# Performance work log

Hardware: AMD Instinct MI355X
Metric: run time of the kernel (lower is better)

The kernel has to match this reference:

```python
import jax, jax.numpy as jnp
from jax import lax
import numpy as np

H = 512       # nhidden
IN = 300      # title/body input dim
TLEN = 40     # title_len
BLEN = 200    # body_len
B = 256       # batch
CH = 512      # classify_hidden
NC = 4        # nclass


def setup_inputs():
    key = jax.random.key(0)
    ks = jax.random.split(key, 17)
    s = 1.0 / np.sqrt(H)
    u = lambda k, sh: jax.random.uniform(k, sh, jnp.float32, -s, s)
    return {
        "x": jax.random.normal(ks[0], (B, TLEN + BLEN, IN), jnp.float32),
        "title_Wih": u(ks[1], (2, 4 * H, IN)),
        "title_Whh": u(ks[2], (2, 4 * H, H)),
        "title_bih": u(ks[3], (2, 4 * H)),
        "title_bhh": u(ks[4], (2, 4 * H)),
        "body_Wih": u(ks[5], (2, 4 * H, IN)),
        "body_Whh": u(ks[6], (2, 4 * H, H)),
        "body_bih": u(ks[7], (2, 4 * H)),
        "body_bhh": u(ks[8], (2, 4 * H)),
        "bil_W": u(ks[9], (1, 2 * H, 2 * H)),
        "bil_b": u(ks[10], (1,)),
        "attn_W": u(ks[11], (2 * H, 4 * H)),
        "attn_b": u(ks[12], (2 * H,)),
        "dec_W": u(ks[13], (CH, 4 * H)),
        "dec_b": u(ks[14], (CH,)),
        "cls_W": u(ks[15], (NC, CH)),
        "cls_b": u(ks[16], (NC,)),
    }


def _lstm_dir(x, Wih, Whh, bih, bhh, h0, c0, reverse):
    # x: [B, T, I]; precompute input-to-gate contributions for all timesteps
    xg = jnp.einsum('bti,gi->btg', x, Wih) + bih + bhh  # [B, T, 4H]

    def step(carry, xg_t):
        h, c = carry
        g = xg_t + h @ Whh.T  # PyTorch gate order: i, f, g, o
        i, f, gg, o = jnp.split(g, 4, axis=-1)
        c = jax.nn.sigmoid(f) * c + jax.nn.sigmoid(i) * jnp.tanh(gg)
        h = jax.nn.sigmoid(o) * jnp.tanh(c)
        return (h, c), h

    (hT, cT), hs = lax.scan(step, (h0, c0), jnp.swapaxes(xg, 0, 1), reverse=reverse)
    return jnp.swapaxes(hs, 0, 1), hT, cT  # outputs aligned to input time order


def _bilstm(x, Wih, Whh, bih, bhh, h0, c0):
    # h0, c0: [2, B, H] (dir 0 = forward, dir 1 = backward)
    out_f, hf, cf = _lstm_dir(x, Wih[0], Whh[0], bih[0], bhh[0], h0[0], c0[0], False)
    out_b, hb, cb = _lstm_dir(x, Wih[1], Whh[1], bih[1], bhh[1], h0[1], c0[1], True)
    out = jnp.concatenate([out_f, out_b], axis=-1)  # [B, T, 2H]
    return out, jnp.stack([hf, hb]), jnp.stack([cf, cb])


def reference(x, title_Wih, title_Whh, title_bih, title_bhh,
              body_Wih, body_Whh, body_bih, body_bhh,
              bil_W, bil_b, attn_W, attn_b, dec_W, dec_b, cls_W, cls_b):
    title, body = x[:, :TLEN, :], x[:, TLEN:, :]
    z = jnp.zeros((2, x.shape[0], H), x.dtype)
    title_out, hn, cn = _bilstm(title, title_Wih, title_Whh, title_bih, title_bhh, z, z)
    # conditional=True: body RNN starts from title final (h, c)
    body_out, _, _ = _bilstm(body, body_Wih, body_Whh, body_bih, body_bhh, hn, cn)
    body_last = body_out[:, -1, :]  # [B, 2H]
    # vectorized bilinear attention over title timesteps (replaces per-t loop)
    scores = jnp.einsum('bte,oeh,bh->bto', title_out, bil_W, body_last) + bil_b
    scores = jax.nn.softmax(scores[..., 0], axis=-1)  # [B, TLEN]
    context = jnp.einsum('bte,bt->be', title_out, scores)  # [B, 2H]
    attn = jnp.tanh(jnp.concatenate([context, body_last], axis=1) @ attn_W.T + attn_b)
    output = jnp.concatenate([title_out[:, -1, :], attn], axis=1)  # [B, 4H]
    class_hidden = output @ dec_W.T + dec_b  # dropout p=0.0 -> identity
    return jax.nn.softmax(class_hidden @ cls_W.T + cls_b, axis=-1)
```

## Files before the change

kernel.cpp:

```cpp
#include <hip/hip_runtime.h>
#include <math.h>

#define HD    512
#define BATCH 256
#define TDIM  240
#define INDIM 300

typedef unsigned short u16;
typedef u16   u16x8 __attribute__((ext_vector_type(8)));
typedef float f32x4 __attribute__((ext_vector_type(4)));

__device__ __forceinline__ u16 bf16_rte(float v) {
    unsigned u = __builtin_bit_cast(unsigned, v);
    unsigned r = (u + 0x7FFFu + ((u >> 16) & 1u)) >> 16;
    return (u16)r;
}

__device__ __forceinline__ void mfma16(f32x4& d, u16x8 a, u16x8 b) {
    asm("v_mfma_f32_16x16x32_bf16 %0, %1, %2, %0" : "+v"(d) : "v"(a), "v"(b));
}

__global__ __launch_bounds__(256) void split_pad(
    const float* __restrict__ src, u16* __restrict__ hi, u16* __restrict__ lo,
    int rows, int kin, int kout)
{
    long i = (long)blockIdx.x * 256 + threadIdx.x;
    if (i >= (long)rows * kout) return;
    int r = (int)(i / kout);
    int k = (int)(i - (long)r * kout);
    float v = (k < kin) ? src[(long)r * kin + k] : 0.f;
    u16 h = bf16_rte(v);
    float hf = __builtin_bit_cast(float, (unsigned)h << 16);
    hi[i] = h;
    lo[i] = bf16_rte(v - hf);
}

struct StepDir {
    const u16* Wih_h; const u16* Wih_l;
    const u16* Whh_h; const u16* Whh_l;
    const float* bih; const float* bhh;
    const u16* hh; const u16* hl;
    u16* oh; u16* ol;
    float* c;
    float* ex; long exs;
    int t;
};

__global__ __launch_bounds__(64) void step_mfma(
    const u16* __restrict__ xh, const u16* __restrict__ xl,
    StepDir d0, StepDir d1)
{
    StepDir D = blockIdx.z ? d1 : d0;
    const int gx   = blockIdx.x;
    const int xcd  = gx & 7, j = gx >> 3;
    const int cblk = xcd * 4 + (j & 3);
    const int rblk = j >> 2;
    const int lane = threadIdx.x;
    const int lr   = lane & 15;
    const int lk8  = (lane >> 4) * 8;
    const int b0   = rblk * 32;
    const int col  = cblk * 16 + lr;

    f32x4 acc[2][4];
    #pragma unroll
    for (int g = 0; g < 4; ++g) {
        float bs = D.bih[g * HD + col] + D.bhh[g * HD + col];
        acc[0][g] = f32x4{bs, bs, bs, bs};
        acc[1][g] = f32x4{bs, bs, bs, bs};
    }

    u16x8 Ah0[2], Al0[2], Bh0[4], Bl0[4];
    u16x8 Ah1[2], Al1[2], Bh1[4], Bl1[4];

    auto MMA = [&](u16x8 (&Ah)[2], u16x8 (&Al)[2], u16x8 (&Bh)[4], u16x8 (&Bl)[4]) {
        #pragma unroll
        for (int rt = 0; rt < 2; ++rt)
            #pragma unroll
            for (int g = 0; g < 4; ++g) {
                mfma16(acc[rt][g], Ah[rt], Bh[g]);
                mfma16(acc[rt][g], Ah[rt], Bl[g]);
                mfma16(acc[rt][g], Al[rt], Bh[g]);
            }
    };

    {
        auto LD = [&](u16x8 (&Ah)[2], u16x8 (&Al)[2], u16x8 (&Bh)[4], u16x8 (&Bl)[4], int ks) {
            const int ko = ks * 32 + lk8;
            #pragma unroll
            for (int rt = 0; rt < 2; ++rt) {
                long off = ((long)(b0 + rt * 16 + lr) * TDIM + D.t) * 320 + ko;
                Ah[rt] = *(const u16x8*)(xh + off);
                Al[rt] = *(const u16x8*)(xl + off);
            }
            #pragma unroll
            for (int g = 0; g < 4; ++g) {
                long off = (long)(g * HD + col) * 320 + ko;
                Bh[g] = *(const u16x8*)(D.Wih_h + off);
                Bl[g] = *(const u16x8*)(D.Wih_l + off);
            }
        };
        LD(Ah0, Al0, Bh0, Bl0, 0);
        #pragma unroll
        for (int ks = 0; ks < 10; ks += 2) {
            LD(Ah1, Al1, Bh1, Bl1, ks + 1);
            MMA(Ah0, Al0, Bh0, Bl0);
            if (ks + 2 < 10) LD(Ah0, Al0, Bh0, Bl0, ks + 2);
            MMA(Ah1, Al1, Bh1, Bl1);
        }
    }
    {
        auto LD = [&](u16x8 (&Ah)[2], u16x8 (&Al)[2], u16x8 (&Bh)[4], u16x8 (&Bl)[4], int ks) {
            const int ko = ks * 32 + lk8;
            #pragma unroll
            for (int rt = 0; rt < 2; ++rt) {
                long off = (long)(b0 + rt * 16 + lr) * HD + ko;
                Ah[rt] = *(const u16x8*)(D.hh + off);
                Al[rt] = *(const u16x8*)(D.hl + off);
            }
            #pragma unroll
            for (int g = 0; g < 4; ++g) {
                long off = (long)(g * HD + col) * HD + ko;
                Bh[g] = *(const u16x8*)(D.Whh_h + off);
                Bl[g] = *(const u16x8*)(D.Whh_l + off);
            }
        };
        LD(Ah0, Al0, Bh0, Bl0, 0);
        #pragma unroll
        for (int ks = 0; ks < 16; ks += 2) {
            LD(Ah1, Al1, Bh1, Bl1, ks + 1);
            MMA(Ah0, Al0, Bh0, Bl0);
            if (ks + 2 < 16) LD(Ah0, Al0, Bh0, Bl0, ks + 2);
            MMA(Ah1, Al1, Bh1, Bl1);
        }
    }

    #pragma unroll
    for (int rt = 0; rt < 2; ++rt) {
        #pragma unroll
        for (int r = 0; r < 4; ++r) {
            const int b = b0 + rt * 16 + (lane >> 4) * 4 + r;
            const long hoff = (long)b * HD + col;
            float iv = acc[rt][0][r];
            float fv = acc[rt][1][r];
            float gv = acc[rt][2][r];
            float ov = acc[rt][3][r];
            float cp = D.c[hoff];
            float si = 1.f / (1.f + expf(-iv));
            float sf = 1.f / (1.f + expf(-fv));
            float so = 1.f / (1.f + expf(-ov));
            float cn = sf * cp + si * tanhf(gv);
            float hn = so * tanhf(cn);
            D.c[hoff] = cn;
            u16 hb = bf16_rte(hn);
            D.oh[hoff] = hb;
            D.ol[hoff] = bf16_rte(hn - __builtin_bit_cast(float, (unsigned)hb << 16));
            if (D.ex) D.ex[(long)b * D.exs + col] = hn;
        }
    }
}

__global__ __launch_bounds__(64) void xg_mfma(
    const u16* __restrict__ xh, const u16* __restrict__ xl,
    const u16* __restrict__ Wih_h, const u16* __restrict__ Wih_l,
    const float* __restrict__ bih, const float* __restrict__ bhh,
    float* __restrict__ xgT, int t0abs, int tstep)
{
    const int bx   = blockIdx.x;
    const int tloc = bx >> 9;
    const int rem  = bx & 511;
    const int rblk = rem >> 6;
    const int cgrp = rem & 63;
    const int lane = threadIdx.x;
    const int lr = lane & 15, lk8 = (lane >> 4) * 8;
    const int b0 = rblk * 32;
    const int tx = t0abs + tstep * tloc;
    const int colf0 = cgrp * 32 + lr;
    const int colf1 = colf0 + 16;

    f32x4 acc[2][2];
    {
        float bs0 = bih[colf0] + bhh[colf0];
        float bs1 = bih[colf1] + bhh[colf1];
        acc[0][0] = f32x4{bs0, bs0, bs0, bs0};
        acc[1][0] = f32x4{bs0, bs0, bs0, bs0};
        acc[0][1] = f32x4{bs1, bs1, bs1, bs1};
        acc[1][1] = f32x4{bs1, bs1, bs1, bs1};
    }

    u16x8 a0h[2], a0l[2], b0h[2], b0l[2];
    u16x8 a1h[2], a1l[2], b1h[2], b1l[2];

    auto LD = [&](u16x8 (&Ah)[2], u16x8 (&Al)[2], u16x8 (&Bh)[2], u16x8 (&Bl)[2], int ks) {
        const int ko = ks * 32 + lk8;
        #pragma unroll
        for (int rt = 0; rt < 2; ++rt) {
            long off = ((long)(b0 + rt * 16 + lr) * TDIM + tx) * 320 + ko;
            Ah[rt] = *(const u16x8*)(xh + off);
            Al[rt] = *(const u16x8*)(xl + off);
        }
        long w0 = (long)colf0 * 320 + ko;
        long w1 = (long)colf1 * 320 + ko;
        Bh[0] = *(const u16x8*)(Wih_h + w0);
        Bl[0] = *(const u16x8*)(Wih_l + w0);
        Bh[1] = *(const u16x8*)(Wih_h + w1);
        Bl[1] = *(const u16x8*)(Wih_l + w1);
    };
    auto MMA = [&](u16x8 (&Ah)[2], u16x8 (&Al)[2], u16x8 (&Bh)[2], u16x8 (&Bl)[2]) {
        #pragma unroll
        for (int rt = 0; rt < 2; ++rt)
            #pragma unroll
            for (int cf = 0; cf < 2; ++cf) {
                mfma16(acc[rt][cf], Ah[rt], Bh[cf]);
                mfma16(acc[rt][cf], Ah[rt], Bl[cf]);
                mfma16(acc[rt][cf], Al[rt], Bh[cf]);
            }
    };

    LD(a0h, a0l, b0h, b0l, 0);
    #pragma unroll
    for (int ks = 0; ks < 10; ks += 2) {
        LD(a1h, a1l, b1h, b1l, ks + 1);
        MMA(a0h, a0l, b0h, b0l);
        if (ks + 2 < 10) LD(a0h, a0l, b0h, b0l, ks + 2);
        MMA(a1h, a1l, b1h, b1l);
    }

    #pragma unroll
    for (int rt = 0; rt < 2; ++rt) {
        long o0 = ((long)tloc * 2048 + colf0) * 256 + b0 + rt * 16 + (lane >> 4) * 4;
        long o1 = ((long)tloc * 2048 + colf1) * 256 + b0 + rt * 16 + (lane >> 4) * 4;
        *(f32x4*)(xgT + o0) = acc[rt][0];
        *(f32x4*)(xgT + o1) = acc[rt][1];
    }
}

__device__ __forceinline__ void group_bar(unsigned* cnt, unsigned* gen,
                                          unsigned nb, unsigned g)
{
    __syncthreads();
    if (threadIdx.x == 0) {
        unsigned old = __hip_atomic_fetch_add(cnt, 1u, __ATOMIC_RELEASE,
                                              __HIP_MEMORY_SCOPE_AGENT);
        if (old == nb - 1u) {
            __hip_atomic_store(cnt, 0u, __ATOMIC_RELAXED, __HIP_MEMORY_SCOPE_AGENT);
            __hip_atomic_store(gen, g + 1u, __ATOMIC_RELEASE, __HIP_MEMORY_SCOPE_AGENT);
        } else {
            while (__hip_atomic_load(gen, __ATOMIC_RELAXED, __HIP_MEMORY_SCOPE_AGENT) < g + 1u)
                __builtin_amdgcn_s_sleep(2);
            (void)__hip_atomic_load(gen, __ATOMIC_ACQUIRE, __HIP_MEMORY_SCOPE_AGENT);
        }
    }
    __syncthreads();
}

__global__ __launch_bounds__(256) void lstm_persist(
    const float* __restrict__ xgT,
    const u16* __restrict__ Whh_h, const u16* __restrict__ Whh_l,
    u16* __restrict__ hAh, u16* __restrict__ hAl,
    u16* __restrict__ hBh, u16* __restrict__ hBl,
    float* __restrict__ cst,
    float* __restrict__ ex, long ex_bstride, int ex_t0, int ex_tstep,
    int ex_coff, int ex_final,
    unsigned* __restrict__ bars, int s0, int L)
{
    const int gx   = blockIdx.x;
    const int xcd  = gx & 7, j = gx >> 3;
    const int cblk = xcd * 4 + (j & 3);
    const int rblk = j >> 2;
    const int wid  = threadIdx.x >> 6;
    const int lane = threadIdx.x & 63;
    const int lr   = lane & 15;
    const int lk8  = (lane >> 4) * 8;
    const int b0   = rblk * 32;
    const int col  = cblk * 16 + lr;

    __shared__ u16 WH[64][520];
    __shared__ u16 WL[64][520];
    __shared__ f32x4 RED[3][64][8];

    for (int idx = threadIdx.x; idx < 64 * 64; idx += 256) {
        int rr = idx >> 6;
        int kk = (idx & 63) << 3;
        int g = rr >> 4, cc = rr & 15;
        long gro = (long)(g * HD + cblk * 16 + cc) * HD + kk;
        *(u16x8*)&WH[rr][kk] = *(const u16x8*)(Whh_h + gro);
        *(u16x8*)&WL[rr][kk] = *(const u16x8*)(Whh_l + gro);
    }
    __syncthreads();

    unsigned* bcnt = bars + rblk * 64;
    unsigned* bgen = bars + 512 + rblk * 64;
    unsigned gen = 0;
    const int ksbase = wid * 4;

    for (int ti = 0; ti < L; ++ti) {
        const int s = s0 + ti;
        const u16* hih = (s & 1) ? hBh : hAh;
        const u16* hil = (s & 1) ? hBl : hAl;
        u16* hoh = (s & 1) ? hAh : hBh;
        u16* hol = (s & 1) ? hAl : hBl;

        f32x4 acc[2][4];
        if (wid == 0) {
            #pragma unroll
            for (int rt = 0; rt < 2; ++rt)
                #pragma unroll
                for (int g = 0; g < 4; ++g) {
                    long o = ((long)ti * 2048 + g * HD + col) * 256
                             + b0 + rt * 16 + (lane >> 4) * 4;
                    acc[rt][g] = *(const f32x4*)(xgT + o);
                }
        } else {
            #pragma unroll
            for (int rt = 0; rt < 2; ++rt)
                #pragma unroll
                for (int g = 0; g < 4; ++g) acc[rt][g] = f32x4{0.f, 0.f, 0.f, 0.f};
        }

        u16x8 Ah0[2], Al0[2], Bh0[4], Bl0[4];
        u16x8 Ah1[2], Al1[2], Bh1[4], Bl1[4];

        auto MMA = [&](u16x8 (&Ah)[2], u16x8 (&Al)[2], u16x8 (&Bh)[4], u16x8 (&Bl)[4]) {
            #pragma unroll
            for (int rt = 0; rt < 2; ++rt)
                #pragma unroll
                for (int g = 0; g < 4; ++g) {
                    mfma16(acc[rt][g], Ah[rt], Bh[g]);
                    mfma16(acc[rt][g], Ah[rt], Bl[g]);
                    mfma16(acc[rt][g], Al[rt], Bh[g]);
                }
        };
        auto LD = [&](u16x8 (&Ah)[2], u16x8 (&Al)[2], u16x8 (&Bh)[4], u16x8 (&Bl)[4], int ks) {
            const int ko = ks * 32 + lk8;
            #pragma unroll
            for (int rt = 0; rt < 2; ++rt) {
                long off = (long)(b0 + rt * 16 + lr) * HD + ko;
                Ah[rt] = *(const u16x8*)(hih + off);
                Al[rt] = *(const u16x8*)(hil + off);
            }
            #pragma unroll
            for (int g = 0; g < 4; ++g) {
                Bh[g] = *(const u16x8*)&WH[g * 16 + lr][ko];
                Bl[g] = *(const u16x8*)&WL[g * 16 + lr][ko];
            }
        };

        LD(Ah0, Al0, Bh0, Bl0, ksbase + 0);
        LD(Ah1, Al1, Bh1, Bl1, ksbase + 1);
        MMA(Ah0, Al0, Bh0, Bl0);
        LD(Ah0, Al0, Bh0, Bl0, ksbase + 2);
        MMA(Ah1, Al1, Bh1, Bl1);
        LD(Ah1, Al1, Bh1, Bl1, ksbase + 3);
        MMA(Ah0, Al0, Bh0, Bl0);
        MMA(Ah1, Al1, Bh1, Bl1);

        if (wid != 0) {
            #pragma unroll
            for (int rt = 0; rt < 2; ++rt)
                #pragma unroll
                for (int g = 0; g < 4; ++g)
                    RED[wid - 1][lane][rt * 4 + g] = acc[rt][g];
        }
        __syncthreads();

        if (wid == 0) {
            #pragma unroll
            for (int w = 0; w < 3; ++w)
                #pragma unroll
                for (int rt = 0; rt < 2; ++rt)
                    #pragma unroll
                    for (int g = 0; g < 4; ++g)
                        acc[rt][g] += RED[w][lane][rt * 4 + g];

            const bool exw = (ex_final == -2) || (ex_final >= 0 && ti == ex_final);
            const int tt = ex_t0 + ex_tstep * ti;
            #pragma unroll
            for (int rt = 0; rt < 2; ++rt) {
                #pragma unroll
                for (int r = 0; r < 4; ++r) {
                    const int b = b0 + rt * 16 + (lane >> 4) * 4 + r;
                    const long hoff = (long)b * HD + col;
                    float iv = acc[rt][0][r];
                    float fv = acc[rt][1][r];
                    float gv = acc[rt][2][r];
                    float ov = acc[rt][3][r];
                    float cp = cst[hoff];
                    float si = 1.f / (1.f + expf(-iv));
                    float sf = 1.f / (1.f + expf(-fv));
                    float so = 1.f / (1.f + expf(-ov));
                    float cn = sf * cp + si * tanhf(gv);
                    float hn = so * tanhf(cn);
                    cst[hoff] = cn;
                    u16 hb = bf16_rte(hn);
                    hoh[hoff] = hb;
                    hol[hoff] = bf16_rte(hn - __builtin_bit_cast(float, (unsigned)hb << 16));
                    if (exw) ex[(long)b * ex_bstride + (long)tt * 1024 + ex_coff + col] = hn;
                }
            }
        }
        if (ti + 1 < L) { group_bar(bcnt, bgen, 32u, gen); ++gen; }
    }
}

__global__ __launch_bounds__(64) void body_persist(
    const u16* __restrict__ xh, const u16* __restrict__ xl,
    const u16* __restrict__ Wih_h, const u16* __restrict__ Wih_l,
    const u16* __restrict__ Whh_h, const u16* __restrict__ Whh_l,
    const float* __restrict__ bih, const float* __restrict__ bhh,
    u16* __restrict__ hAh, u16* __restrict__ hAl,
    u16* __restrict__ hBh, u16* __restrict__ hBl,
    float* __restrict__ cst, float* __restrict__ ex,
    unsigned* __restrict__ bars)
{
    const int gx   = blockIdx.x;
    const int xcd  = gx & 7, j = gx >> 3;
    const int cblk = xcd * 4 + (j & 3);
    const int rblk = j >> 2;
    const int lane = threadIdx.x;
    const int lr   = lane & 15;
    const int lk8  = (lane >> 4) * 8;
    const int b0   = rblk * 32;
    const int col  = cblk * 16 + lr;

    __shared__ u16 WH[64][520];
    __shared__ u16 WL[64][520];
    for (int idx = lane; idx < 64 * 64; idx += 64) {
        int rr = idx >> 6;
        int kk = (idx & 63) << 3;
        int g = rr >> 4, cc = rr & 15;
        long gro = (long)(g * HD + cblk * 16 + cc) * HD + kk;
        *(u16x8*)&WH[rr][kk] = *(const u16x8*)(Whh_h + gro);
        *(u16x8*)&WL[rr][kk] = *(const u16x8*)(Whh_l + gro);
    }
    __syncthreads();

    float bsum[4];
    #pragma unroll
    for (int g = 0; g < 4; ++g) bsum[g] = bih[g * HD + col] + bhh[g * HD + col];

    unsigned* bcnt = bars + rblk * 64;
    unsigned* bgen = bars + 512 + rblk * 64;
    unsigned gen = 0;

    for (int t = 1; t < 200; ++t) {
        const int s = 40 + t;
        const u16* hih = (s & 1) ? hBh : hAh;
        const u16* hil = (s & 1) ? hBl : hAl;
        u16* hoh = (s & 1) ? hAh : hBh;
        u16* hol = (s & 1) ? hAl : hBl;

        f32x4 acc[2][4];
        #pragma unroll
        for (int g = 0; g < 4; ++g) {
            acc[0][g] = f32x4{bsum[g], bsum[g], bsum[g], bsum[g]};
            acc[1][g] = f32x4{bsum[g], bsum[g], bsum[g], bsum[g]};
        }

        u16x8 Ah0[2], Al0[2], Bh0[4], Bl0[4];
        u16x8 Ah1[2], Al1[2], Bh1[4], Bl1[4];

        auto MMA = [&](u16x8 (&Ah)[2], u16x8 (&Al)[2], u16x8 (&Bh)[4], u16x8 (&Bl)[4]) {
            #pragma unroll
            for (int rt = 0; rt < 2; ++rt)
                #pragma unroll
                for (int g = 0; g < 4; ++g) {
                    mfma16(acc[rt][g], Ah[rt], Bh[g]);
                    mfma16(acc[rt][g], Ah[rt], Bl[g]);
                    mfma16(acc[rt][g], Al[rt], Bh[g]);
                }
        };
        {
            auto LD = [&](u16x8 (&Ah)[2], u16x8 (&Al)[2], u16x8 (&Bh)[4], u16x8 (&Bl)[4], int ks) {
                const int ko = ks * 32 + lk8;
                #pragma unroll
                for (int rt = 0; rt < 2; ++rt) {
                    long off = ((long)(b0 + rt * 16 + lr) * TDIM + (40 + t)) * 320 + ko;
                    Ah[rt] = *(const u16x8*)(xh + off);
                    Al[rt] = *(const u16x8*)(xl + off);
                }
                #pragma unroll
                for (int g = 0; g < 4; ++g) {
                    long off = (long)(g * HD + col) * 320 + ko;
                    Bh[g] = *(const u16x8*)(Wih_h + off);
                    Bl[g] = *(const u16x8*)(Wih_l + off);
                }
            };
            LD(Ah0, Al0, Bh0, Bl0, 0);
            #pragma unroll
            for (int ks = 0; ks < 10; ks += 2) {
                LD(Ah1, Al1, Bh1, Bl1, ks + 1);
                MMA(Ah0, Al0, Bh0, Bl0);
                if (ks + 2 < 10) LD(Ah0, Al0, Bh0, Bl0, ks + 2);
                MMA(Ah1, Al1, Bh1, Bl1);
            }
        }
        {
            auto LD = [&](u16x8 (&Ah)[2], u16x8 (&Al)[2], u16x8 (&Bh)[4], u16x8 (&Bl)[4], int ks) {
                const int ko = ks * 32 + lk8;
                #pragma unroll
                for (int rt = 0; rt < 2; ++rt) {
                    long off = (long)(b0 + rt * 16 + lr) * HD + ko;
                    Ah[rt] = *(const u16x8*)(hih + off);
                    Al[rt] = *(const u16x8*)(hil + off);
                }
                #pragma unroll
                for (int g = 0; g < 4; ++g) {
                    Bh[g] = *(const u16x8*)&WH[g * 16 + lr][ko];
                    Bl[g] = *(const u16x8*)&WL[g * 16 + lr][ko];
                }
            };
            LD(Ah0, Al0, Bh0, Bl0, 0);
            #pragma unroll
            for (int ks = 0; ks < 16; ks += 2) {
                LD(Ah1, Al1, Bh1, Bl1, ks + 1);
                MMA(Ah0, Al0, Bh0, Bl0);
                if (ks + 2 < 16) LD(Ah0, Al0, Bh0, Bl0, ks + 2);
                MMA(Ah1, Al1, Bh1, Bl1);
            }
        }
        float* exw = (t == 199) ? ex : (float*)nullptr;
        #pragma unroll
        for (int rt = 0; rt < 2; ++rt) {
            #pragma unroll
            for (int r = 0; r < 4; ++r) {
                const int b = b0 + rt * 16 + (lane >> 4) * 4 + r;
                const long hoff = (long)b * HD + col;
                float iv = acc[rt][0][r];
                float fv = acc[rt][1][r];
                float gv = acc[rt][2][r];
                float ov = acc[rt][3][r];
                float cp = cst[hoff];
                float si = 1.f / (1.f + expf(-iv));
                float sf = 1.f / (1.f + expf(-fv));
                float so = 1.f / (1.f + expf(-ov));
                float cn = sf * cp + si * tanhf(gv);
                float hn = so * tanhf(cn);
                cst[hoff] = cn;
                u16 hb = bf16_rte(hn);
                hoh[hoff] = hb;
                hol[hoff] = bf16_rte(hn - __builtin_bit_cast(float, (unsigned)hb << 16));
                if (exw) exw[(long)b * 1024 + col] = hn;
            }
        }
        group_bar(bcnt, bgen, 32u, gen);
        ++gen;
    }
}

template<int ACT>
__global__ __launch_bounds__(64) void mfma_gemm(
    const u16* __restrict__ Ah_, const u16* __restrict__ Al_,
    const u16* __restrict__ Wh_, const u16* __restrict__ Wl_,
    const float* __restrict__ bias, float* __restrict__ C,
    int ldc, int K, int n16)
{
    const int gx = blockIdx.x;
    const int nblk = gx % n16, mblk = gx / n16;
    const int lane = threadIdx.x;
    const int lr = lane & 15, lk8 = (lane >> 4) * 8;
    const int b0 = mblk * 32, col = nblk * 16 + lr;

    f32x4 acc[2] = {f32x4{0,0,0,0}, f32x4{0,0,0,0}};
    u16x8 A0[2], L0[2], A1[2], L1[2];
    u16x8 B0, M0, B1, M1;

    auto LD = [&](u16x8 (&A)[2], u16x8 (&L)[2], u16x8& B, u16x8& M, int ks) {
        const int ko = ks * 32 + lk8;
        #pragma unroll
        for (int rt = 0; rt < 2; ++rt) {
            long off = (long)(b0 + rt * 16 + lr) * K + ko;
            A[rt] = *(const u16x8*)(Ah_ + off);
            L[rt] = *(const u16x8*)(Al_ + off);
        }
        long woff = (long)col * K + ko;
        B = *(const u16x8*)(Wh_ + woff);
        M = *(const u16x8*)(Wl_ + woff);
    };
    auto MMA = [&](u16x8 (&A)[2], u16x8 (&L)[2], u16x8& B, u16x8& M) {
        #pragma unroll
        for (int rt = 0; rt < 2; ++rt) {
            mfma16(acc[rt], A[rt], B);
            mfma16(acc[rt], A[rt], M);
            mfma16(acc[rt], L[rt], B);
        }
    };

    const int NS = K >> 5;
    LD(A0, L0, B0, M0, 0);
    for (int ks = 0; ks < NS; ks += 2) {
        if (ks + 1 < NS) LD(A1, L1, B1, M1, ks + 1);
        MMA(A0, L0, B0, M0);
        if (ks + 2 < NS) LD(A0, L0, B0, M0, ks + 2);
        if (ks + 1 < NS) MMA(A1, L1, B1, M1);
    }

    float bs = bias ? bias[col] : 0.f;
    #pragma unroll
    for (int rt = 0; rt < 2; ++rt)
        #pragma unroll
        for (int r = 0; r < 4; ++r) {
            int m = b0 + rt * 16 + (lane >> 4) * 4 + r;
            float v = acc[rt][r] + bs;
            if (ACT == 1) v = tanhf(v);
            C[(long)m * ldc + col] = v;
        }
}

template<int BB>
__global__ __launch_bounds__(256) void lstm_step(
    const float* __restrict__ x,
    const float* __restrict__ Wih0, const float* __restrict__ Whh0,
    const float* __restrict__ bih0, const float* __restrict__ bhh0,
    const float* __restrict__ hin0, float* __restrict__ hnew0, float* __restrict__ cst0,
    float* __restrict__ ex0, int exs0, int tx0,
    const float* __restrict__ Wih1, const float* __restrict__ Whh1,
    const float* __restrict__ bih1, const float* __restrict__ bhh1,
    const float* __restrict__ hin1, float* __restrict__ hnew1, float* __restrict__ cst1,
    float* __restrict__ ex1, int exs1, int tx1)
{
    const int dir = blockIdx.z;
    const float* Wih = dir ? Wih1 : Wih0;
    const float* Whh = dir ? Whh1 : Whh0;
    const float* bih = dir ? bih1 : bih0;
    const float* bhh = dir ? bhh1 : bhh0;
    const float* hin = dir ? hin1 : hin0;
    float* hnew = dir ? hnew1 : hnew0;
    float* cst  = dir ? cst1  : cst0;
    float* ex   = dir ? ex1   : ex0;
    const int exs = dir ? exs1 : exs0;
    const int tx  = dir ? tx1  : tx0;

    const int bblk = blockIdx.x, kblk = blockIdx.y;
    const int tid = threadIdx.x;
    const int j  = tid & 15;
    const int ty = tid >> 4;
    const int k  = kblk * 16 + j;
    constexpr int RB = BB / 16;

    __shared__ float As[BB][33];
    __shared__ float Bs[32][65];

    float acc[RB][4];
    #pragma unroll
    for (int r = 0; r < RB; ++r)
        #pragma unroll
        for (int q = 0; q < 4; ++q) acc[r][q] = 0.f;

    const int lb = tid >> 5, lk = tid & 31;

    for (int kb = 0; kb < INDIM; kb += 32) {
        #pragma unroll
        for (int it = 0; it < BB/8; ++it) {
            int b = lb + it*8;
            int i = kb + lk;
            As[b][lk] = (i < INDIM) ? x[((bblk*BB + b)*TDIM + tx)*INDIM + i] : 0.f;
        }
        #pragma unroll
        for (int it = 0; it < 8; ++it) {
            int col = lb + it*8;
            int g = (col >> 4)*HD + kblk*16 + (col & 15);
            int i = kb + lk;
            Bs[lk][col] = (i < INDIM) ? Wih[g*INDIM + i] : 0.f;
        }
        __syncthreads();
        #pragma unroll
        for (int kk = 0; kk < 32; ++kk) {
            float a_[RB], b_[4];
            #pragma unroll
            for (int r = 0; r < RB; ++r) a_[r] = As[ty*RB + r][kk];
            #pragma unroll
            for (int q = 0; q < 4; ++q) b_[q] = Bs[kk][q*16 + j];
            #pragma unroll
            for (int r = 0; r < RB; ++r)
                #pragma unroll
                for (int q = 0; q < 4; ++q) acc[r][q] += a_[r]*b_[q];
        }
        __syncthreads();
    }
    for (int kb = 0; kb < HD; kb += 32) {
        #pragma unroll
        for (int it = 0; it < BB/8; ++it) {
            int b = lb + it*8;
            As[b][lk] = hin[(bblk*BB + b)*HD + kb + lk];
        }
        #pragma unroll
        for (int it = 0; it < 8; ++it) {
            int col = lb + it*8;
            int g = (col >> 4)*HD + kblk*16 + (col & 15);
            Bs[lk][col] = Whh[g*HD + kb + lk];
        }
        __syncthreads();
        #pragma unroll
        for (int kk = 0; kk < 32; ++kk) {
            float a_[RB], b_[4];
            #pragma unroll
            for (int r = 0; r < RB; ++r) a_[r] = As[ty*RB + r][kk];
            #pragma unroll
            for (int q = 0; q < 4; ++q) b_[q] = Bs[kk][q*16 + j];
            #pragma unroll
            for (int r = 0; r < RB; ++r)
                #pragma unroll
                for (int q = 0; q < 4; ++q) acc[r][q] += a_[r]*b_[q];
        }
        __syncthreads();
    }
    float bsum[4];
    #pragma unroll
    for (int q = 0; q < 4; ++q) bsum[q] = bih[q*HD + k] + bhh[q*HD + k];
    #pragma unroll
    for (int r = 0; r < RB; ++r) {
        int gb = bblk*BB + ty*RB + r;
        float iv = acc[r][0] + bsum[0];
        float fv = acc[r][1] + bsum[1];
        float gv = acc[r][2] + bsum[2];
        float ov = acc[r][3] + bsum[3];
        float cprev = cst[gb*HD + k];
        float si = 1.f/(1.f + expf(-iv));
        float sf = 1.f/(1.f + expf(-fv));
        float so = 1.f/(1.f + expf(-ov));
        float cn = sf*cprev + si*tanhf(gv);
        float hn = so*tanhf(cn);
        cst[gb*HD + k]  = cn;
        hnew[gb*HD + k] = hn;
        if (ex) ex[gb*exs + k] = hn;
    }
}

template<int ACT>
__global__ __launch_bounds__(256) void gemm_bias_act(
    const float* __restrict__ A, int lda,
    const float* __restrict__ W,
    const float* __restrict__ bias,
    float* __restrict__ C, int ldc,
    int K)
{
    const int mblk = blockIdx.x, nblk = blockIdx.y;
    const int tid = threadIdx.x;
    const int txd = tid & 15, ty = tid >> 4;
    __shared__ float As[32][33];
    __shared__ float Bs[32][65];
    float acc[2][4] = {{0.f,0.f,0.f,0.f},{0.f,0.f,0.f,0.f}};
    const int lb = tid >> 5, lk = tid & 31;

    for (int kb = 0; kb < K; kb += 32) {
        #pragma unroll
        for (int it = 0; it < 4; ++it) {
            int r = lb + it*8;
            As[r][lk] = A[(mblk*32 + r)*lda + kb + lk];
        }
        #pragma unroll
        for (int it = 0; it < 8; ++it) {
            int col = lb + it*8;
            Bs[lk][col] = W[(nblk*64 + col)*K + kb + lk];
        }
        __syncthreads();
        #pragma unroll
        for (int kk = 0; kk < 32; ++kk) {
            float a0 = As[ty*2 + 0][kk], a1 = As[ty*2 + 1][kk];
            float b_[4];
            #pragma unroll
            for (int q = 0; q < 4; ++q) b_[q] = Bs[kk][q*16 + txd];
            #pragma unroll
            for (int q = 0; q < 4; ++q) { acc[0][q] += a0*b_[q]; acc[1][q] += a1*b_[q]; }
        }
        __syncthreads();
    }
    #pragma unroll
    for (int r = 0; r < 2; ++r) {
        int m = mblk*32 + ty*2 + r;
        #pragma unroll
        for (int q = 0; q < 4; ++q) {
            int n = nblk*64 + q*16 + txd;
            float v = acc[r][q] + (bias ? bias[n] : 0.f);
            if (ACT == 1) v = tanhf(v);
            C[m*ldc + n] = v;
        }
    }
}

__global__ __launch_bounds__(256) void attn_ctx(
    const float* __restrict__ title_out,
    const float* __restrict__ u,
    const float* __restrict__ bilb,
    float* __restrict__ attn_in)
{
    int b = blockIdx.x;
    int tid = threadIdx.x;
    __shared__ float uL[1024];
    __shared__ float sc[40];
    for (int e = tid; e < 1024; e += 256) uL[e] = u[b*1024 + e];
    __syncthreads();
    int wave = tid >> 6, lane = tid & 63;
    for (int t = wave*10; t < wave*10 + 10; ++t) {
        const float* row = title_out + (b*40 + t)*1024;
        float s = 0.f;
        for (int e = lane; e < 1024; e += 64) s += row[e]*uL[e];
        #pragma unroll
        for (int off = 32; off > 0; off >>= 1) s += __shfl_down(s, off, 64);
        if (lane == 0) sc[t] = s + bilb[0];
    }
    __syncthreads();
    if (tid < 64) {
        float v = (tid < 40) ? sc[tid] : -1e30f;
        float m = v;
        #pragma unroll
        for (int off = 32; off > 0; off >>= 1) m = fmaxf(m, __shfl_xor(m, off, 64));
        float e = (tid < 40) ? expf(v - m) : 0.f;
        float ssum = e;
        #pragma unroll
        for (int off = 32; off > 0; off >>= 1) ssum += __shfl_xor(ssum, off, 64);
        if (tid < 40) sc[tid] = e / ssum;
    }
    __syncthreads();
    for (int e = tid; e < 1024; e += 256) {
        float a = 0.f;
        #pragma unroll
        for (int t = 0; t < 40; ++t) a += sc[t]*title_out[(b*40 + t)*1024 + e];
        attn_in[b*2048 + e] = a;
    }
}

__global__ void copy_rows(const float* __restrict__ src, int ss,
                          float* __restrict__ dst, int ds, int n)
{
    int b = blockIdx.x;
    for (int e = threadIdx.x; e < n; e += blockDim.x) dst[b*ds + e] = src[b*ss + e];
}

__global__ __launch_bounds__(64) void final_cls(
    const float* __restrict__ ch,
    const float* __restrict__ clsW,
    const float* __restrict__ clsb,
    float* __restrict__ out)
{
    int b = blockIdx.x*64 + threadIdx.x;
    float o[4];
    #pragma unroll
    for (int n = 0; n < 4; ++n) {
        float s = clsb[n];
        for (int jj = 0; jj < 512; ++jj) s += ch[b*512 + jj]*clsW[n*512 + jj];
        o[n] = s;
    }
    float m = fmaxf(fmaxf(o[0], o[1]), fmaxf(o[2], o[3]));
    float e0 = expf(o[0]-m), e1 = expf(o[1]-m), e2 = expf(o[2]-m), e3 = expf(o[3]-m);
    float s = e0 + e1 + e2 + e3;
    out[b*4+0] = e0/s; out[b*4+1] = e1/s; out[b*4+2] = e2/s; out[b*4+3] = e3/s;
}

extern "C" void kernel_launch(void* const* d_in, const int* in_sizes, int n_in,
                              void* d_out, int out_size, void* d_ws, size_t ws_size,
                              hipStream_t stream) {
    const float* x     = (const float*)d_in[0];
    const float* tWih  = (const float*)d_in[1];
    const float* tWhh  = (const float*)d_in[2];
    const float* tbih  = (const float*)d_in[3];
    const float* tbhh  = (const float*)d_in[4];
    const float* bWih  = (const float*)d_in[5];
    const float* bWhh  = (const float*)d_in[6];
    const float* bbih  = (const float*)d_in[7];
    const float* bbhh  = (const float*)d_in[8];
    const float* bilW  = (const float*)d_in[9];
    const float* bilb  = (const float*)d_in[10];
    const float* attnW = (const float*)d_in[11];
    const float* attnb = (const float*)d_in[12];
    const float* decW  = (const float*)d_in[13];
    const float* decb  = (const float*)d_in[14];
    const float* clsW  = (const float*)d_in[15];
    const float* clsb  = (const float*)d_in[16];

    char* base = (char*)d_ws;
    size_t off = 0;
    auto carve = [&](size_t bytes) -> void* {
        void* r = base + off; off += (bytes + 255) & ~(size_t)255; return r;
    };

    u16* hA0h = (u16*)carve(BATCH*HD*2);
    u16* hA0l = (u16*)carve(BATCH*HD*2);
    u16* hA1h = (u16*)carve(BATCH*HD*2);
    u16* hA1l = (u16*)carve(BATCH*HD*2);
    float* c0 = (float*)carve(BATCH*HD*4);
    float* c1 = (float*)carve(BATCH*HD*4);
    unsigned* bars = (unsigned*)carve(32*4096);
    size_t zero_bytes = off;
    u16* hB0h = (u16*)carve(BATCH*HD*2);
    u16* hB0l = (u16*)carve(BATCH*HD*2);
    u16* hB1h = (u16*)carve(BATCH*HD*2);
    u16* hB1l = (u16*)carve(BATCH*HD*2);
    u16* xh = (u16*)carve((size_t)BATCH*TDIM*320*2);
    u16* xl = (u16*)carve((size_t)BATCH*TDIM*320*2);
    u16* tW0ih_h = (u16*)carve(2048*320*2); u16* tW0ih_l = (u16*)carve(2048*320*2);
    u16* tW1ih_h = (u16*)carve(2048*320*2); u16* tW1ih_l = (u16*)carve(2048*320*2);
    u16* bW0ih_h = (u16*)carve(2048*320*2); u16* bW0ih_l = (u16*)carve(2048*320*2);
    u16* bW1ih_h = (u16*)carve(2048*320*2); u16* bW1ih_l = (u16*)carve(2048*320*2);
    u16* tW0hh_h = (u16*)carve(2048*512*2); u16* tW0hh_l = (u16*)carve(2048*512*2);
    u16* tW1hh_h = (u16*)carve(2048*512*2); u16* tW1hh_l = (u16*)carve(2048*512*2);
    u16* bW0hh_h = (u16*)carve(2048*512*2); u16* bW0hh_l = (u16*)carve(2048*512*2);
    u16* bW1hh_h = (u16*)carve(2048*512*2); u16* bW1hh_l = (u16*)carve(2048*512*2);
    float* title_out = (float*)carve((size_t)BATCH*40*1024*4);
    float* body_last = (float*)carve((size_t)BATCH*1024*4);
    float* u_buf     = (float*)carve((size_t)BATCH*1024*4);
    float* attn_in   = (float*)carve((size_t)BATCH*2048*4);
    float* out_cat   = (float*)carve((size_t)BATCH*2048*4);
    float* ch        = (float*)carve((size_t)BATCH*512*4);
    u16* bl_h = (u16*)carve((size_t)BATCH*1024*2); u16* bl_l = (u16*)carve((size_t)BATCH*1024*2);
    u16* ai_h = (u16*)carve((size_t)BATCH*2048*2); u16* ai_l = (u16*)carve((size_t)BATCH*2048*2);
    u16* oc_h = (u16*)carve((size_t)BATCH*2048*2); u16* oc_l = (u16*)carve((size_t)BATCH*2048*2);
    u16* bilW_h  = (u16*)carve(1024*1024*2); u16* bilW_l  = (u16*)carve(1024*1024*2);
    u16* attnW_h = (u16*)carve((size_t)1024*2048*2); u16* attnW_l = (u16*)carve((size_t)1024*2048*2);
    u16* decW_h  = (u16*)carve((size_t)512*2048*2);  u16* decW_l  = (u16*)carve((size_t)512*2048*2);
    size_t need = off;

    const size_t SLAB_BYTES = (size_t)2048 * 256 * 4;
    float* xgT = (float*)(base + off);
    int C = 0;
    if (ws_size > need) {
        size_t nslab = (ws_size - need) / SLAB_BYTES;
        C = (int)(nslab > 50 ? 50 : nslab);
    }
    const bool xg_ok = (C >= 10);

    if (ws_size >= need) {
        hipMemsetAsync(d_ws, 0, zero_bytes, stream);

        auto SPLIT = [&](const float* s, u16* h, u16* l, long rows, int kin, int kout) {
            long n = rows * (long)kout;
            split_pad<<<dim3((unsigned)((n + 255) / 256)), 256, 0, stream>>>(s, h, l, (int)rows, kin, kout);
        };
        SPLIT(x, xh, xl, (long)BATCH*TDIM, INDIM, 320);
        SPLIT(tWih,               tW0ih_h, tW0ih_l, 2048, INDIM, 320);
        SPLIT(tWih + 2048*INDIM,  tW1ih_h, tW1ih_l, 2048, INDIM, 320);
        SPLIT(bWih,               bW0ih_h, bW0ih_l, 2048, INDIM, 320);
        SPLIT(bWih + 2048*INDIM,  bW1ih_h, bW1ih_l, 2048, INDIM, 320);
        SPLIT(tWhh,               tW0hh_h, tW0hh_l, 2048, HD, HD);
        SPLIT(tWhh + 2048*HD,     tW1hh_h, tW1hh_l, 2048, HD, HD);
        SPLIT(bWhh,               bW0hh_h, bW0hh_l, 2048, HD, HD);
        SPLIT(bWhh + 2048*HD,     bW1hh_h, bW1hh_l, 2048, HD, HD);
        SPLIT(bilW,  bilW_h,  bilW_l,  1024, 1024, 1024);
        SPLIT(attnW, attnW_h, attnW_l, 1024, 2048, 2048);
        SPLIT(decW,  decW_h,  decW_l,  512,  2048, 2048);

        if (xg_ok) {
            int ci = 0;
            for (int tb = 0; tb < 40; tb += C, ++ci) {
                int L = (C < 40 - tb) ? C : (40 - tb);
                xg_mfma<<<dim3((unsigned)(L*512)), 64, 0, stream>>>(
                    xh, xl, tW0ih_h, tW0ih_l, tbih, tbhh, xgT, tb, 1);
                lstm_persist<<<dim3(256), 256, 0, stream>>>(
                    xgT, tW0hh_h, tW0hh_l, hA0h, hA0l, hB0h, hB0l, c0,
                    title_out, 40*1024, tb, 1, 0, -2,
                    bars + (size_t)ci*1024, tb, L);
            }
            for (int tb = 0; tb < 40; tb += C, ++ci) {
                int L = (C < 40 - tb) ? C : (40 - tb);
                xg_mfma<<<dim3((unsigned)(L*512)), 64, 0, stream>>>(
                    xh, xl, tW1ih_h, tW1ih_l, tbih + 2048, tbhh + 2048, xgT, 39 - tb, -1);
                lstm_persist<<<dim3(256), 256, 0, stream>>>(
                    xgT, tW1hh_h, tW1hh_l, hA1h, hA1l, hB1h, hB1l, c1,
                    title_out, 40*1024, 39 - tb, -1, 512, -2,
                    bars + (size_t)ci*1024, tb, L);
            }
            {
                StepDir F = { bW0ih_h, bW0ih_l, bW0hh_h, bW0hh_l, bbih, bbhh,
                              hA0h, hA0l, hB0h, hB0l, c0, (float*)nullptr, 0, 40 };
                StepDir R = { bW1ih_h, bW1ih_l, bW1hh_h, bW1hh_l, bbih + 2048, bbhh + 2048,
                              hA1h, hA1l, hB1h, hB1l, c1, body_last + 512, 1024, 239 };
                step_mfma<<<dim3(256,1,2), 64, 0, stream>>>(xh, xl, F, R);
            }
            for (int tb = 1; tb < 200; tb += C, ++ci) {
                int L = (C < 200 - tb) ? C : (200 - tb);
                bool last = (tb + L == 200);
                xg_mfma<<<dim3((unsigned)(L*512)), 64, 0, stream>>>(
                    xh, xl, bW0ih_h, bW0ih_l, bbih, bbhh, xgT, 40 + tb, 1);
                lstm_persist<<<dim3(256), 256, 0, stream>>>(
                    xgT, bW0hh_h, bW0hh_l, hA0h, hA0l, hB0h, hB0l, c0,
                    body_last, 1024, 0, 0, 0, last ? (L - 1) : -1,
                    bars + (size_t)ci*1024, 40 + tb, L);
            }
        } else {
            for (int t = 0; t < 40; ++t) {
                bool odd = t & 1;
                StepDir A = { tW0ih_h, tW0ih_l, tW0hh_h, tW0hh_l, tbih, tbhh,
                              odd?hB0h:hA0h, odd?hB0l:hA0l, odd?hA0h:hB0h, odd?hA0l:hB0l,
                              c0, title_out + (size_t)t*1024, 40*1024, t };
                StepDir B = { tW1ih_h, tW1ih_l, tW1hh_h, tW1hh_l, tbih + 2048, tbhh + 2048,
                              odd?hB1h:hA1h, odd?hB1l:hA1l, odd?hA1h:hB1h, odd?hA1l:hB1l,
                              c1, title_out + (size_t)(39 - t)*1024 + 512, 40*1024, 39 - t };
                step_mfma<<<dim3(256,1,2), 64, 0, stream>>>(xh, xl, A, B);
            }
            {
                StepDir F = { bW0ih_h, bW0ih_l, bW0hh_h, bW0hh_l, bbih, bbhh,
                              hA0h, hA0l, hB0h, hB0l, c0, (float*)nullptr, 0, 40 };
                StepDir R = { bW1ih_h, bW1ih_l, bW1hh_h, bW1hh_l, bbih + 2048, bbhh + 2048,
                              hA1h, hA1l, hB1h, hB1l, c1, body_last + 512, 1024, 239 };
                step_mfma<<<dim3(256,1,2), 64, 0, stream>>>(xh, xl, F, R);
            }
            body_persist<<<dim3(256), 64, 0, stream>>>(
                xh, xl, bW0ih_h, bW0ih_l, bW0hh_h, bW0hh_l, bbih, bbhh,
                hA0h, hA0l, hB0h, hB0l, c0, body_last, bars);
        }

        SPLIT(body_last, bl_h, bl_l, 256, 1024, 1024);
        mfma_gemm<0><<<dim3(8*64), 64, 0, stream>>>(bl_h, bl_l, bilW_h, bilW_l,
                                                    (const float*)nullptr, u_buf, 1024, 1024, 64);
        attn_ctx<<<256, 256, 0, stream>>>(title_out, u_buf, bilb, attn_in);
        copy_rows<<<256, 256, 0, stream>>>(body_last, 1024, attn_in + 1024, 2048, 1024);
        copy_rows<<<256, 256, 0, stream>>>(title_out + 39*1024, 40*1024, out_cat, 2048, 1024);
        SPLIT(attn_in, ai_h, ai_l, 256, 2048, 2048);
        mfma_gemm<1><<<dim3(8*64), 64, 0, stream>>>(ai_h, ai_l, attnW_h, attnW_l,
                                                    attnb, out_cat + 1024, 2048, 2048, 64);
        SPLIT(out_cat, oc_h, oc_l, 256, 2048, 2048);
        mfma_gemm<0><<<dim3(8*32), 64, 0, stream>>>(oc_h, oc_l, decW_h, decW_l,
                                                    decb, ch, 512, 2048, 32);
        final_cls<<<4, 64, 0, stream>>>(ch, clsW, clsb, (float*)d_out);
    } else {
        float* p = (float*)d_ws;
        float* lhA0 = p; p += BATCH*HD;
        float* lc0  = p; p += BATCH*HD;
        float* lhA1 = p; p += BATCH*HD;
        float* lc1  = p; p += BATCH*HD;
        float* lhB0 = p; p += BATCH*HD;
        float* lhB1 = p; p += BATCH*HD;
        float* l_title = p; p += (size_t)BATCH*40*1024;
        float* l_blast = p; p += BATCH*1024;
        float* l_u     = p; p += BATCH*1024;
        float* l_ain   = p; p += BATCH*2048;
        float* l_ocat  = p; p += BATCH*2048;
        float* l_ch    = p; p += BATCH*512;

        hipMemsetAsync(lhA0, 0, (size_t)4*BATCH*HD*sizeof(float), stream);
        const float* tWih1 = tWih + 2048*INDIM;
        const float* tWhh1 = tWhh + 2048*HD;
        const float* bWih1 = bWih + 2048*INDIM;
        const float* bWhh1 = bWhh + 2048*HD;

        for (int t = 0; t < 40; ++t) {
            float* hi0 = (t & 1) ? lhB0 : lhA0;
            float* ho0 = (t & 1) ? lhA0 : lhB0;
            float* hi1 = (t & 1) ? lhB1 : lhA1;
            float* ho1 = (t & 1) ? lhA1 : lhB1;
            lstm_step<64><<<dim3(4,32,2), 256, 0, stream>>>(
                x, tWih, tWhh, tbih, tbhh, hi0, ho0, lc0,
                l_title + t*1024, 40*1024, t,
                tWih1, tWhh1, tbih + 2048, tbhh + 2048, hi1, ho1, lc1,
                l_title + (39 - t)*1024 + 512, 40*1024, 39 - t);
        }
        lstm_step<64><<<dim3(4,32,2), 256, 0, stream>>>(
            x, bWih, bWhh, bbih, bbhh, lhA0, lhB0, lc0, (float*)nullptr, 0, 40,
            bWih1, bWhh1, bbih + 2048, bbhh + 2048, lhA1, lhB1, lc1, l_blast + 512, 1024, 239);
        for (int t = 1; t < 200; ++t) {
            int s = 40 + t;
            float* hi = (s & 1) ? lhB0 : lhA0;
            float* ho = (s & 1) ? lhA0 : lhB0;
            float* exp_ = (t == 199) ? l_blast : (float*)nullptr;
            lstm_step<32><<<dim3(8,32,1), 256, 0, stream>>>(
                x, bWih, bWhh, bbih, bbhh, hi, ho, lc0, exp_, 1024, 40 + t,
                nullptr, nullptr, nullptr, nullptr, nullptr, nullptr, nullptr,
                (float*)nullptr, 0, 0);
        }
        gemm_bias_act<0><<<dim3(8,16), 256, 0, stream>>>(l_blast, 1024, bilW, nullptr, l_u, 1024, 1024);
        attn_ctx<<<256, 256, 0, stream>>>(l_title, l_u, bilb, l_ain);
        copy_rows<<<256, 256, 0, stream>>>(l_blast, 1024, l_ain + 1024, 2048, 1024);
        copy_rows<<<256, 256, 0, stream>>>(l_title + 39*1024, 40*1024, l_ocat, 2048, 1024);
        gemm_bias_act<1><<<dim3(8,16), 256, 0, stream>>>(l_ain, 2048, attnW, attnb, l_ocat + 1024, 2048, 2048);
        gemm_bias_act<0><<<dim3(8,8), 256, 0, stream>>>(l_ocat, 2048, decW, decb, l_ch, 512, 2048);
        final_cls<<<4, 64, 0, stream>>>(l_ch, clsW, clsb, (float*)d_out);
    }
}
```

Baseline: 5.779 ms.

## Keep LSTM cell state in registers, prefetch next-step gate inputs, remap blocks

The persistent LSTM kernel now keeps cell state in registers across timesteps and writes it back to global memory only on the last step, which removes a global load and store per element per step. The precomputed input-gate slab for step ti+1 is prefetched with nontemporal loads while step ti computes, hiding load latency behind the barrier and MMA work. Block-to-tile mapping changes from an XCD-aware layout to a plain row-major split, which alters which blocks share L2 and which blocks meet at each group barrier. The maximum number of xg slabs grows from 50 to 200, so fewer chunk launches are needed at the cost of more workspace.

```diff
diff --git a/kernel.cpp b/kernel.cpp
--- a/kernel.cpp
+++ b/kernel.cpp
@@ -264,9 +264,8 @@
     unsigned* __restrict__ bars, int s0, int L)
 {
     const int gx   = blockIdx.x;
-    const int xcd  = gx & 7, j = gx >> 3;
-    const int cblk = xcd * 4 + (j & 3);
-    const int rblk = j >> 2;
+    const int rblk = gx & 7;
+    const int cblk = gx >> 3;
     const int wid  = threadIdx.x >> 6;
     const int lane = threadIdx.x & 63;
     const int lr   = lane & 15;
@@ -293,6 +292,24 @@
     unsigned gen = 0;
     const int ksbase = wid * 4;
 
+    f32x4 creg[2];
+    f32x4 nxt[2][4];
+    if (wid == 0) {
+        #pragma unroll
+        for (int rt = 0; rt < 2; ++rt)
+            #pragma unroll
+            for (int r = 0; r < 4; ++r)
+                creg[rt][r] = cst[(long)(b0 + rt * 16 + (lane >> 4) * 4 + r) * HD + col];
+        #pragma unroll
+        for (int rt = 0; rt < 2; ++rt)
+            #pragma unroll
+            for (int g = 0; g < 4; ++g) {
+                long o = ((long)0 * 2048 + g * HD + col) * 256
+                         + b0 + rt * 16 + (lane >> 4) * 4;
+                nxt[rt][g] = __builtin_nontemporal_load((const f32x4*)(xgT + o));
+            }
+    }
+
     for (int ti = 0; ti < L; ++ti) {
         const int s = s0 + ti;
         const u16* hih = (s & 1) ? hBh : hAh;
@@ -305,11 +322,17 @@
             #pragma unroll
             for (int rt = 0; rt < 2; ++rt)
                 #pragma unroll
-                for (int g = 0; g < 4; ++g) {
-                    long o = ((long)ti * 2048 + g * HD + col) * 256
-                             + b0 + rt * 16 + (lane >> 4) * 4;
-                    acc[rt][g] = *(const f32x4*)(xgT + o);
-                }
+                for (int g = 0; g < 4; ++g) acc[rt][g] = nxt[rt][g];
+            if (ti + 1 < L) {
+                #pragma unroll
+                for (int rt = 0; rt < 2; ++rt)
+                    #pragma unroll
+                    for (int g = 0; g < 4; ++g) {
+                        long o = ((long)(ti + 1) * 2048 + g * HD + col) * 256
+                                 + b0 + rt * 16 + (lane >> 4) * 4;
+                        nxt[rt][g] = __builtin_nontemporal_load((const f32x4*)(xgT + o));
+                    }
+            }
         } else {
             #pragma unroll
             for (int rt = 0; rt < 2; ++rt)
@@ -373,6 +396,7 @@
                         acc[rt][g] += RED[w][lane][rt * 4 + g];
 
             const bool exw = (ex_final == -2) || (ex_final >= 0 && ti == ex_final);
+            const bool lastti = (ti == L - 1);
             const int tt = ex_t0 + ex_tstep * ti;
             #pragma unroll
             for (int rt = 0; rt < 2; ++rt) {
@@ -384,17 +408,18 @@
                     float fv = acc[rt][1][r];
                     float gv = acc[rt][2][r];
                     float ov = acc[rt][3][r];
-                    float cp = cst[hoff];
+                    float cp = creg[rt][r];
                     float si = 1.f / (1.f + expf(-iv));
                     float sf = 1.f / (1.f + expf(-fv));
                     float so = 1.f / (1.f + expf(-ov));
                     float cn = sf * cp + si * tanhf(gv);
                     float hn = so * tanhf(cn);
-                    cst[hoff] = cn;
+                    creg[rt][r] = cn;
                     u16 hb = bf16_rte(hn);
                     hoh[hoff] = hb;
                     hol[hoff] = bf16_rte(hn - __builtin_bit_cast(float, (unsigned)hb << 16));
                     if (exw) ex[(long)b * ex_bstride + (long)tt * 1024 + ex_coff + col] = hn;
+                    if (lastti) cst[hoff] = cn;
                 }
             }
         }
@@ -915,7 +940,7 @@
     int C = 0;
     if (ws_size > need) {
         size_t nslab = (ws_size - need) / SLAB_BYTES;
-        C = (int)(nslab > 50 ? 50 : nslab);
+        C = (int)(nslab > 200 ? 200 : nslab);
     }
     const bool xg_ok = (C >= 10);
 
```

New measurement: 5.323 ms. -7.9%, faster.
